# Performance work log

Measured on AMD Instinct MI355X. Metric: run time of the kernel, lower is better.

Reference implementation:

```python
import jax, jax.numpy as jnp
import numpy as np

B, DIM_X, K = 16384, 2048, 128


def setup_inputs() -> dict:
    key = jax.random.key(0)
    k_x, k_y, k_z, k_ew, k_eb, k_dw = jax.random.split(key, 6)
    x = jax.random.normal(k_x, (B, DIM_X), dtype=jnp.float32)
    # targets are +/-1 (sign labels, matching sign(y_hat)==y accuracy check)
    y = jnp.sign(jax.random.normal(k_y, (B,), dtype=jnp.float32))
    y = jnp.where(y == 0, 1.0, y)
    z = jax.random.randint(k_z, (B,), 0, K)
    # torch.nn.Linear default init: U(-1/sqrt(fan_in), 1/sqrt(fan_in))
    be = 1.0 / np.sqrt(DIM_X)
    enc_W = jax.random.uniform(k_ew, (K, DIM_X), jnp.float32, -be, be)
    enc_b = jax.random.uniform(k_eb, (K,), jnp.float32, -be, be)
    # torch.nn.Bilinear weight shape [out=1, in1=K, in2=DIM_X], U(-1/sqrt(in1), 1/sqrt(in1))
    bd = 1.0 / np.sqrt(K)
    dec_W = jax.random.uniform(k_dw, (1, K, DIM_X), jnp.float32, -bd, bd)
    dec_bias = jnp.zeros((K,), dtype=jnp.float32)
    return {"x": x, "y": y, "z": z, "enc_W": enc_W, "enc_b": enc_b,
            "dec_W": dec_W, "dec_bias": dec_bias}


def reference(x, y, z, enc_W, enc_b, dec_W, dec_bias):
    # encoder: single Linear (num_layers=1)
    s = x @ enc_W.T + enc_b                      # [B, K]
    # argmax_onehot: hard one-hot routing (eval mode, no gumbel)
    z_hat_index = jnp.argmax(s, axis=-1)          # [B]
    z_tilde = jax.nn.one_hot(z_hat_index, s.shape[-1], dtype=s.dtype)  # [B, K]
    # Bilinear(K, dim_X, 1, bias=False) + z_tilde @ decoder_bias
    y_hat = jnp.einsum('bk,kd,bd->b', z_tilde, dec_W[0], x) + z_tilde @ dec_bias
    loss = jnp.mean(jnp.square(y_hat - y))
    accuracy = jnp.mean((jnp.sign(y_hat) == y).astype(jnp.float32))
    return (y_hat, z_hat_index, loss, accuracy)
```

## Files before the change

### kernel.cpp

```cpp
#include <hip/hip_runtime.h>

#define BB 16384
#define DD 2048
#define KK 128
#define NT 64
#define NCHK 32
#define RPB 64
#define NBLK 256
#define DELTA 8e-3f
#define BUFS 49152
#define FCAP 2048

typedef __attribute__((ext_vector_type(8))) short  bf16x8;
typedef __attribute__((ext_vector_type(4))) float  f32x4;
typedef __attribute__((ext_vector_type(4))) unsigned int u32x4;

union V16 { u32x4 u; f32x4 f; bf16x8 s; };

__device__ __forceinline__ void gld16(const void* g, void* l) {
  __builtin_amdgcn_global_load_lds(
      (const __attribute__((address_space(1))) void*)g,
      (__attribute__((address_space(3))) void*)l, 16, 0, 0);
}

__global__ __launch_bounds__(256) void prep_kernel(
    const float* __restrict__ encW, const float* __restrict__ decW,
    unsigned short* __restrict__ wEh, unsigned short* __restrict__ wDh,
    float* __restrict__ out, unsigned int* __restrict__ counter)
{
  __shared__ float sw[16][260];
  const int bid = blockIdx.x;
  const int tid = threadIdx.x;
  if (bid == 0 && tid == 0) { *counter = 0u; out[2*BB] = 0.f; out[2*BB+1] = 0.f; }
  const int sel = bid >> 6, rem = bid & 63;
  const int ct = rem >> 3, kt = rem & 7;
  const float* W = sel ? decW : encW;
  unsigned short* oh = sel ? wDh : wEh;

  {
    const int row = tid >> 4, seg = tid & 15;
    const float* src = W + (size_t)(ct * 16 + row) * DD + kt * 256 + seg * 16;
#pragma unroll
    for (int i = 0; i < 4; ++i)
      *(f32x4*)&sw[row][seg * 16 + i * 4] = *(const f32x4*)(src + i * 4);
  }
  __syncthreads();

  const int l = tid & 63, wv = tid >> 6;
#pragma unroll
  for (int h = 0; h < 2; ++h) {
    const int tt = wv * 2 + h;
    const int t  = kt * 8 + tt;
    const float* sp = &sw[l & 15][tt * 32 + ((l >> 4) << 3)];
    V16 vh;
#pragma unroll
    for (int p = 0; p < 4; ++p) {
      unsigned hu[2];
#pragma unroll
      for (int q = 0; q < 2; ++q) {
        unsigned u  = __float_as_uint(sp[p * 2 + q]);
        unsigned rh = u + 0x7FFFu + ((u >> 16) & 1u);
        hu[q] = (rh >> 16) & 0xFFFFu;
      }
      vh.u[p] = (hu[1] << 16) | hu[0];
    }
    *(u32x4*)(oh + ((size_t)(t * 8 + ct) * 64 + l) * 8) = vh.u;
  }
}

__global__ __launch_bounds__(512)
void main_kernel(
    const float* __restrict__ x, const float* __restrict__ y,
    const float* __restrict__ encb, const float* __restrict__ decb,
    const unsigned short* __restrict__ wEh, const unsigned short* __restrict__ wDh,
    float* __restrict__ out, unsigned int* __restrict__ counter,
    float* __restrict__ list)
{
  __shared__ __align__(16) unsigned char pool[98304];
  const int tid = threadIdx.x;
  const int w = tid >> 6, l = tid & 63;
  const int wr = w >> 2, wcg = w & 3;
  const int rbase = blockIdx.x * RPB;

  const int srow = tid >> 3, seg = tid & 7;
  const float* gXc = x + (size_t)(rbase + srow) * DD + seg * 8;
  const int woff = srow * 128 + ((seg ^ (srow & 7)) << 4);

  int rowb[2];
#pragma unroll
  for (int rt = 0; rt < 2; ++rt)
    rowb[rt] = (wr * 32 + rt * 16 + (l & 15)) * 128;
  int blkb[2];
#pragma unroll
  for (int tt = 0; tt < 2; ++tt)
    blkb[tt] = ((tt * 4 + (l >> 4)) ^ (l & 7)) << 4;

  const int bfo = wcg * 2048 + (l << 4);

  f32x4 accE[2][2], accD[2][2];
  const f32x4 zero4 = {0.f, 0.f, 0.f, 0.f};
#pragma unroll
  for (int rt = 0; rt < 2; ++rt)
#pragma unroll
    for (int ct = 0; ct < 2; ++ct) { accE[rt][ct] = zero4; accD[rt][ct] = zero4; }

  auto WRX = [&](int nb, f32x4 A, f32x4 Bv) {
    float fa[8] = {A[0],A[1],A[2],A[3],Bv[0],Bv[1],Bv[2],Bv[3]};
    V16 vh, vl;
#pragma unroll
    for (int p = 0; p < 4; ++p) {
      unsigned u0 = __float_as_uint(fa[2*p]);
      unsigned u1 = __float_as_uint(fa[2*p+1]);
      vh.u[p] = (u0 >> 16) | (u1 & 0xFFFF0000u);
      float r0 = fa[2*p]   - __uint_as_float(u0 & 0xFFFF0000u);
      float r1 = fa[2*p+1] - __uint_as_float(u1 & 0xFFFF0000u);
      vl.u[p] = (__float_as_uint(r0) >> 16) | (__float_as_uint(r1) & 0xFFFF0000u);
    }
    unsigned char* bp = pool + nb + woff;
    *(u32x4*)bp           = vh.u;
    *(u32x4*)(bp + 8192)  = vl.u;
  };

  auto DMAB = [&](int nb, int c) {
    const unsigned short* eb = wEh + (size_t)(2 * c) * 4096 + tid * 8;
    const unsigned short* db = wDh + (size_t)(2 * c) * 4096 + tid * 8;
    gld16(eb,        pool + nb + 16384 + w * 1024);
    gld16(eb + 4096, pool + nb + 24576 + w * 1024);
    gld16(db,        pool + nb + 32768 + w * 1024);
    gld16(db + 4096, pool + nb + 40960 + w * 1024);
  };

#define MFMA(a, b, c) __builtin_amdgcn_mfma_f32_16x16x32_bf16(a, b, c, 0, 0, 0)
#define KSTEP(cbase, tt) do {                                                    \
    const unsigned char* bp = pool + (cbase);                                    \
    const unsigned char* bb = bp + 16384 + (tt) * 8192 + bfo;                    \
    bf16x8 E0 = *(const bf16x8*)bb;                                              \
    bf16x8 E1 = *(const bf16x8*)(bb + 1024);                                     \
    bf16x8 D0 = *(const bf16x8*)(bb + 16384);                                    \
    bf16x8 D1 = *(const bf16x8*)(bb + 16384 + 1024);                             \
    _Pragma("unroll")                                                            \
    for (int rt = 0; rt < 2; ++rt) {                                             \
      const unsigned char* ap = bp + rowb[rt] + blkb[tt];                        \
      bf16x8 ah = *(const bf16x8*)ap;                                            \
      bf16x8 al = *(const bf16x8*)(ap + 8192);                                   \
      accE[rt][0] = MFMA(ah, E0, accE[rt][0]);                                   \
      accE[rt][1] = MFMA(ah, E1, accE[rt][1]);                                   \
      accD[rt][0] = MFMA(ah, D0, accD[rt][0]);                                   \
      accD[rt][1] = MFMA(ah, D1, accD[rt][1]);                                   \
      accE[rt][0] = MFMA(al, E0, accE[rt][0]);                                   \
      accE[rt][1] = MFMA(al, E1, accE[rt][1]);                                   \
    }                                                                            \
  } while (0)

  {
    f32x4 xA = *(const f32x4*)gXc;
    f32x4 xB = *(const f32x4*)(gXc + 4);
    DMAB(0, 0);
    WRX(0, xA, xB);
    asm volatile("s_waitcnt vmcnt(0) lgkmcnt(0)" ::: "memory");
    __builtin_amdgcn_s_barrier();
  }

  for (int c = 0; c < NCHK; ++c) {
    const int cb = (c & 1) * BUFS;
    const int nb = cb ^ BUFS;
    f32x4 xA, xB;
    if (c + 1 < NCHK) {
      const float* p = gXc + (size_t)(c + 1) * 64;
      xA = *(const f32x4*)p; xB = *(const f32x4*)(p + 4);
      DMAB(nb, c + 1);
    }
    __builtin_amdgcn_s_setprio(1);
    KSTEP(cb, 0);
    KSTEP(cb, 1);
    __builtin_amdgcn_s_setprio(0);
    if (c + 1 < NCHK) WRX(nb, xA, xB);
    asm volatile("s_waitcnt vmcnt(0) lgkmcnt(0)" ::: "memory");
    __builtin_amdgcn_s_barrier();
  }
#undef KSTEP
#undef MFMA

  float* sT  = (float*)pool;
  float* sS  = (float*)(pool + 33792);
  float* sm1 = (float*)(pool + 66560);
  float* sm2 = (float*)(pool + 67584);
  int*   si1 = (int*)  (pool + 68608);

  {
    const int q = l >> 4, cc = l & 15;
    const int col0 = wcg * 32 + cc;
    const int col1 = col0 + 16;
#pragma unroll
    for (int rt = 0; rt < 2; ++rt)
#pragma unroll
      for (int ct = 0; ct < 2; ++ct) {
        const int col = wcg * 32 + ct * 16 + cc;
#pragma unroll
        for (int i = 0; i < 4; ++i)
          sT[(wr * 32 + rt * 16 + q * 4 + i) * 132 + col] = accD[rt][ct][i];
      }
    const float b0 = encb[col0], b1 = encb[col1];
    float m1v[8], m2v[8]; int i1v[8];
#pragma unroll
    for (int rt = 0; rt < 2; ++rt)
#pragma unroll
      for (int i = 0; i < 4; ++i) {
        const int j = rt * 4 + i;
        const int row = wr * 32 + rt * 16 + q * 4 + i;
        float v0 = accE[rt][0][i] + b0;
        float v1 = accE[rt][1][i] + b1;
        sS[row * 128 + col0] = v0;
        sS[row * 128 + col1] = v1;
        if (v0 >= v1) { m1v[j] = v0; m2v[j] = v1; i1v[j] = col0; }
        else          { m1v[j] = v1; m2v[j] = v0; i1v[j] = col1; }
      }
#pragma unroll
    for (int d = 1; d < 16; d <<= 1) {
#pragma unroll
      for (int j = 0; j < 8; ++j) {
        float om1 = __shfl_xor(m1v[j], d);
        float om2 = __shfl_xor(m2v[j], d);
        int   oi  = __shfl_xor(i1v[j], d);
        if (om1 > m1v[j] || (om1 == m1v[j] && oi < i1v[j])) {
          m2v[j] = fmaxf(m1v[j], om2); m1v[j] = om1; i1v[j] = oi;
        } else {
          m2v[j] = fmaxf(m2v[j], om1);
        }
      }
    }
    if (cc == 0) {
#pragma unroll
      for (int rt = 0; rt < 2; ++rt)
#pragma unroll
        for (int i = 0; i < 4; ++i) {
          const int j = rt * 4 + i;
          const int row = wr * 32 + rt * 16 + q * 4 + i;
          sm1[row * 4 + wcg] = m1v[j];
          sm2[row * 4 + wcg] = m2v[j];
          si1[row * 4 + wcg] = i1v[j];
        }
    }
  }
  __syncthreads();

  float lossAcc = 0.f, accAcc = 0.f;
  if (tid < RPB) {
    const int row = tid, R = rbase + row;
    float m1 = -3.4e38f, m2 = -3.4e38f; int i1 = 0;
#pragma unroll
    for (int g = 0; g < 4; ++g) {
      float a1 = sm1[row * 4 + g], a2 = sm2[row * 4 + g];
      int ai = si1[row * 4 + g];
      if (a1 > m1) { m2 = fmaxf(m1, a2); m1 = a1; i1 = ai; }
      else         { m2 = fmaxf(m2, a1); }
    }
    float yh = sT[row * 132 + i1] + decb[i1];
    out[R]      = yh;
    out[BB + R] = (float)i1;
    if (m1 - m2 < DELTA) {
      unsigned p = atomicAdd(counter, 1u);
      if (p < (unsigned)FCAP) {
        float* ent = list + (size_t)p * 132;
        ((unsigned*)ent)[0] = (unsigned)R;
        const f32x4* sr = (const f32x4*)(sS + row * 128);
        f32x4* dst = (f32x4*)(ent + 4);
#pragma unroll
        for (int j = 0; j < 32; ++j) dst[j] = sr[j];
      }
    }
    float yv = y[R];
    float d  = yh - yv;
    lossAcc = d * d;
    float sg = (yh > 0.f) ? 1.f : ((yh < 0.f) ? -1.f : 0.f);
    accAcc = (sg == yv) ? 1.f : 0.f;
  }
#pragma unroll
  for (int d = 1; d < 64; d <<= 1) {
    lossAcc += __shfl_xor(lossAcc, d);
    accAcc  += __shfl_xor(accAcc, d);
  }
  if (tid == 0) {
    atomicAdd(&out[2*BB],     lossAcc * (1.f / BB));
    atomicAdd(&out[2*BB + 1], accAcc  * (1.f / BB));
  }
}

__global__ __launch_bounds__(64) void fixup_kernel(
    const float* __restrict__ x, const float* __restrict__ y,
    const float* __restrict__ encW, const float* __restrict__ encb,
    const float* __restrict__ decW, const float* __restrict__ decb,
    float* __restrict__ out,
    const unsigned int* __restrict__ counter, const float* __restrict__ list)
{
  int n = (int)*counter;
  if (n > FCAP) n = FCAP;
  const int l = threadIdx.x;
  for (int e = blockIdx.x; e < n; e += gridDim.x) {
    const float* ent = list + (size_t)e * 132;
    const int R = (int)((const unsigned*)ent)[0];
    const float s0 = ent[4 + 2 * l], s1 = ent[5 + 2 * l];
    float m = fmaxf(s0, s1);
#pragma unroll
    for (int d = 1; d < 64; d <<= 1) m = fmaxf(m, __shfl_xor(m, d));
    const float win = m - 2.0f * DELTA;
    unsigned long long mm0 = __ballot(s0 >= win);
    unsigned long long mm1 = __ballot(s1 >= win);
    const float* xr = x + (size_t)R * DD;
    double best = -1e300; int bk = KK;
    while (mm0 | mm1) {
      int c;
      if (mm0) { int b = __builtin_ctzll(mm0); mm0 &= mm0 - 1; c = 2 * b; }
      else     { int b = __builtin_ctzll(mm1); mm1 &= mm1 - 1; c = 2 * b + 1; }
      const float* wp = encW + (size_t)c * DD;
      double s = 0.0;
#pragma unroll
      for (int j = 0; j < 8; ++j) {
        f32x4 wv = *(const f32x4*)(wp + j * 256 + l * 4);
        f32x4 xv = *(const f32x4*)(xr + j * 256 + l * 4);
        s = fma((double)xv[0], (double)wv[0], s);
        s = fma((double)xv[1], (double)wv[1], s);
        s = fma((double)xv[2], (double)wv[2], s);
        s = fma((double)xv[3], (double)wv[3], s);
      }
#pragma unroll
      for (int d = 1; d < 64; d <<= 1) s += __shfl_xor(s, d);
      s += (double)encb[c];
      if (s > best || (s == best && c < bk)) { best = s; bk = c; }
    }
    const float* dr = decW + (size_t)bk * DD;
    double t = 0.0;
#pragma unroll
    for (int j = 0; j < 8; ++j) {
      f32x4 wv = *(const f32x4*)(dr + j * 256 + l * 4);
      f32x4 xv = *(const f32x4*)(xr + j * 256 + l * 4);
      t = fma((double)xv[0], (double)wv[0], t);
      t = fma((double)xv[1], (double)wv[1], t);
      t = fma((double)xv[2], (double)wv[2], t);
      t = fma((double)xv[3], (double)wv[3], t);
    }
#pragma unroll
    for (int d = 1; d < 64; d <<= 1) t += __shfl_xor(t, d);
    if (l == 0) {
      float yh = (float)(t + (double)decb[bk]);
      float yv = y[R];
      float old = out[R];
      float dn = yh - yv, dol = old - yv;
      atomicAdd(&out[2*BB], (dn*dn - dol*dol) * (1.f / BB));
      float sgn = (yh  > 0.f) ? 1.f : ((yh  < 0.f) ? -1.f : 0.f);
      float sgo = (old > 0.f) ? 1.f : ((old < 0.f) ? -1.f : 0.f);
      float mn = (sgn == yv) ? 1.f : 0.f;
      float mo = (sgo == yv) ? 1.f : 0.f;
      atomicAdd(&out[2*BB + 1], (mn - mo) * (1.f / BB));
      out[R]      = yh;
      out[BB + R] = (float)bk;
    }
  }
}

extern "C" void kernel_launch(void* const* d_in, const int* in_sizes, int n_in,
                              void* d_out, int out_size, void* d_ws, size_t ws_size,
                              hipStream_t stream)
{
  const float* x    = (const float*)d_in[0];
  const float* y    = (const float*)d_in[1];
  const float* encW = (const float*)d_in[3];
  const float* encb = (const float*)d_in[4];
  const float* decW = (const float*)d_in[5];
  const float* decb = (const float*)d_in[6];
  float* out = (float*)d_out;

  unsigned char* ws = (unsigned char*)d_ws;
  unsigned short* wEh = (unsigned short*)ws;
  unsigned short* wDh = (unsigned short*)(ws + 524288);
  unsigned int* counter = (unsigned int*)(ws + 1048576);
  float* list = (float*)(ws + 1048592);

  prep_kernel<<<128, 256, 0, stream>>>(encW, decW, wEh, wDh, out, counter);
  main_kernel<<<NBLK, 512, 0, stream>>>(x, y, encb, decb, wEh, wDh,
                                        out, counter, list);
  fixup_kernel<<<512, 64, 0, stream>>>(x, y, encW, encb, decW, decb,
                                       out, counter, list);
}
```

Baseline: 84.02 us.

## Halve K-chunk per pipeline stage and shrink LDS buffers with padded x layout

The main loop now walks 64 chunks of 32 columns instead of 32 chunks of 64, so each double-buffered stage holds half the x and weight data. LDS use drops from 96KB to about 69KB. The XOR swizzle is replaced by an 80-byte padded row stride, and each thread loads 4 floats of x instead of 8. This aims to cut LDS footprint, possibly improving occupancy, and to simplify addressing. In exchange it doubles the number of barriers and waitcnt stalls, and each stage has less work to hide latency behind.

```diff
diff --git a/kernel.cpp b/kernel.cpp
--- a/kernel.cpp
+++ b/kernel.cpp
@@ -4,16 +4,16 @@
 #define DD 2048
 #define KK 128
 #define NT 64
-#define NCHK 32
 #define RPB 64
 #define NBLK 256
 #define DELTA 8e-3f
-#define BUFS 49152
+#define BUFS 26624
 #define FCAP 2048
 
 typedef __attribute__((ext_vector_type(8))) short  bf16x8;
 typedef __attribute__((ext_vector_type(4))) float  f32x4;
 typedef __attribute__((ext_vector_type(4))) unsigned int u32x4;
+typedef __attribute__((ext_vector_type(2))) unsigned int u32x2;
 
 union V16 { u32x4 u; f32x4 f; bf16x8 s; };
 
@@ -76,26 +76,26 @@
     float* __restrict__ out, unsigned int* __restrict__ counter,
     float* __restrict__ list)
 {
-  __shared__ __align__(16) unsigned char pool[98304];
+  __shared__ __align__(16) unsigned char pool[70656];
   const int tid = threadIdx.x;
   const int w = tid >> 6, l = tid & 63;
   const int wr = w >> 2, wcg = w & 3;
   const int rbase = blockIdx.x * RPB;
 
   const int srow = tid >> 3, seg = tid & 7;
-  const float* gXc = x + (size_t)(rbase + srow) * DD + seg * 8;
-  const int woff = srow * 128 + ((seg ^ (srow & 7)) << 4);
+  const float* gXc = x + (size_t)(rbase + srow) * DD + seg * 4;
+  const int xwoff = srow * 80 + seg * 8;
+
+  const unsigned short* gE = wEh + (size_t)tid * 8;
+  const unsigned short* gD = wDh + (size_t)tid * 8;
+  const int dmadst = w * 1024;
 
   int rowb[2];
 #pragma unroll
   for (int rt = 0; rt < 2; ++rt)
-    rowb[rt] = (wr * 32 + rt * 16 + (l & 15)) * 128;
-  int blkb[2];
-#pragma unroll
-  for (int tt = 0; tt < 2; ++tt)
-    blkb[tt] = ((tt * 4 + (l >> 4)) ^ (l & 7)) << 4;
-
-  const int bfo = wcg * 2048 + (l << 4);
+    rowb[rt] = (wr * 32 + rt * 16 + (l & 15)) * 80 + ((l >> 4) << 4);
+
+  const int ebo = 10240 + wcg * 2048 + l * 16;
 
   f32x4 accE[2][2], accD[2][2];
   const f32x4 zero4 = {0.f, 0.f, 0.f, 0.f};
@@ -104,45 +104,40 @@
 #pragma unroll
     for (int ct = 0; ct < 2; ++ct) { accE[rt][ct] = zero4; accD[rt][ct] = zero4; }
 
-  auto WRX = [&](int nb, f32x4 A, f32x4 Bv) {
-    float fa[8] = {A[0],A[1],A[2],A[3],Bv[0],Bv[1],Bv[2],Bv[3]};
-    V16 vh, vl;
-#pragma unroll
-    for (int p = 0; p < 4; ++p) {
-      unsigned u0 = __float_as_uint(fa[2*p]);
-      unsigned u1 = __float_as_uint(fa[2*p+1]);
-      vh.u[p] = (u0 >> 16) | (u1 & 0xFFFF0000u);
-      float r0 = fa[2*p]   - __uint_as_float(u0 & 0xFFFF0000u);
-      float r1 = fa[2*p+1] - __uint_as_float(u1 & 0xFFFF0000u);
-      vl.u[p] = (__float_as_uint(r0) >> 16) | (__float_as_uint(r1) & 0xFFFF0000u);
-    }
-    unsigned char* bp = pool + nb + woff;
-    *(u32x4*)bp           = vh.u;
-    *(u32x4*)(bp + 8192)  = vl.u;
+  auto DMAB = [&](int nb, int t) {
+    gld16(gE + (size_t)t * 4096, pool + nb + 10240 + dmadst);
+    gld16(gD + (size_t)t * 4096, pool + nb + 18432 + dmadst);
   };
-
-  auto DMAB = [&](int nb, int c) {
-    const unsigned short* eb = wEh + (size_t)(2 * c) * 4096 + tid * 8;
-    const unsigned short* db = wDh + (size_t)(2 * c) * 4096 + tid * 8;
-    gld16(eb,        pool + nb + 16384 + w * 1024);
-    gld16(eb + 4096, pool + nb + 24576 + w * 1024);
-    gld16(db,        pool + nb + 32768 + w * 1024);
-    gld16(db + 4096, pool + nb + 40960 + w * 1024);
+  auto WRX = [&](int nb, f32x4 A) {
+    unsigned u0 = __float_as_uint(A[0]);
+    unsigned u1 = __float_as_uint(A[1]);
+    unsigned u2 = __float_as_uint(A[2]);
+    unsigned u3 = __float_as_uint(A[3]);
+    u32x2 hi, lo;
+    hi[0] = (u0 >> 16) | (u1 & 0xFFFF0000u);
+    hi[1] = (u2 >> 16) | (u3 & 0xFFFF0000u);
+    float r0 = A[0] - __uint_as_float(u0 & 0xFFFF0000u);
+    float r1 = A[1] - __uint_as_float(u1 & 0xFFFF0000u);
+    float r2 = A[2] - __uint_as_float(u2 & 0xFFFF0000u);
+    float r3 = A[3] - __uint_as_float(u3 & 0xFFFF0000u);
+    lo[0] = (__float_as_uint(r0) >> 16) | (__float_as_uint(r1) & 0xFFFF0000u);
+    lo[1] = (__float_as_uint(r2) >> 16) | (__float_as_uint(r3) & 0xFFFF0000u);
+    unsigned char* bp = pool + nb + xwoff;
+    *(u32x2*)bp          = hi;
+    *(u32x2*)(bp + 5120) = lo;
   };
 
 #define MFMA(a, b, c) __builtin_amdgcn_mfma_f32_16x16x32_bf16(a, b, c, 0, 0, 0)
-#define KSTEP(cbase, tt) do {                                                    \
-    const unsigned char* bp = pool + (cbase);                                    \
-    const unsigned char* bb = bp + 16384 + (tt) * 8192 + bfo;                    \
-    bf16x8 E0 = *(const bf16x8*)bb;                                              \
-    bf16x8 E1 = *(const bf16x8*)(bb + 1024);                                     \
-    bf16x8 D0 = *(const bf16x8*)(bb + 16384);                                    \
-    bf16x8 D1 = *(const bf16x8*)(bb + 16384 + 1024);                             \
+#define KSTEP(cb) do {                                                           \
+    const unsigned char* bp = pool + (cb);                                       \
+    bf16x8 E0 = *(const bf16x8*)(bp + ebo);                                      \
+    bf16x8 E1 = *(const bf16x8*)(bp + ebo + 1024);                               \
+    bf16x8 D0 = *(const bf16x8*)(bp + ebo + 8192);                               \
+    bf16x8 D1 = *(const bf16x8*)(bp + ebo + 8192 + 1024);                        \
     _Pragma("unroll")                                                            \
     for (int rt = 0; rt < 2; ++rt) {                                             \
-      const unsigned char* ap = bp + rowb[rt] + blkb[tt];                        \
-      bf16x8 ah = *(const bf16x8*)ap;                                            \
-      bf16x8 al = *(const bf16x8*)(ap + 8192);                                   \
+      bf16x8 ah = *(const bf16x8*)(bp + rowb[rt]);                               \
+      bf16x8 al = *(const bf16x8*)(bp + rowb[rt] + 5120);                        \
       accE[rt][0] = MFMA(ah, E0, accE[rt][0]);                                   \
       accE[rt][1] = MFMA(ah, E1, accE[rt][1]);                                   \
       accD[rt][0] = MFMA(ah, D0, accD[rt][0]);                                   \
@@ -154,27 +149,24 @@
 
   {
     f32x4 xA = *(const f32x4*)gXc;
-    f32x4 xB = *(const f32x4*)(gXc + 4);
     DMAB(0, 0);
-    WRX(0, xA, xB);
+    WRX(0, xA);
     asm volatile("s_waitcnt vmcnt(0) lgkmcnt(0)" ::: "memory");
     __builtin_amdgcn_s_barrier();
   }
 
-  for (int c = 0; c < NCHK; ++c) {
-    const int cb = (c & 1) * BUFS;
+  for (int t = 0; t < NT; ++t) {
+    const int cb = (t & 1) * BUFS;
     const int nb = cb ^ BUFS;
-    f32x4 xA, xB;
-    if (c + 1 < NCHK) {
-      const float* p = gXc + (size_t)(c + 1) * 64;
-      xA = *(const f32x4*)p; xB = *(const f32x4*)(p + 4);
-      DMAB(nb, c + 1);
+    f32x4 xA;
+    if (t + 1 < NT) {
+      DMAB(nb, t + 1);
+      xA = *(const f32x4*)(gXc + (size_t)(t + 1) * 32);
     }
     __builtin_amdgcn_s_setprio(1);
-    KSTEP(cb, 0);
-    KSTEP(cb, 1);
+    KSTEP(cb);
     __builtin_amdgcn_s_setprio(0);
-    if (c + 1 < NCHK) WRX(nb, xA, xB);
+    if (t + 1 < NT) WRX(nb, xA);
     asm volatile("s_waitcnt vmcnt(0) lgkmcnt(0)" ::: "memory");
     __builtin_amdgcn_s_barrier();
   }
@@ -250,10 +242,10 @@
     float m1 = -3.4e38f, m2 = -3.4e38f; int i1 = 0;
 #pragma unroll
     for (int g = 0; g < 4; ++g) {
-      float a1 = sm1[row * 4 + g], a2 = sm2[row * 4 + g];
+      float a1g = sm1[row * 4 + g], a2g = sm2[row * 4 + g];
       int ai = si1[row * 4 + g];
-      if (a1 > m1) { m2 = fmaxf(m1, a2); m1 = a1; i1 = ai; }
-      else         { m2 = fmaxf(m2, a1); }
+      if (a1g > m1) { m2 = fmaxf(m1, a2g); m1 = a1g; i1 = ai; }
+      else          { m2 = fmaxf(m2, a1g); }
     }
     float yh = sT[row * 132 + i1] + decb[i1];
     out[R]      = yh;
```

After: 88.33 us. 5.1% more time.
